# Optimization experiments

Hardware: AMD Instinct MI355X
Metric: run time of the kernel (lower is better)

Reference implementation:

```python
import jax, jax.numpy as jnp
import numpy as np


def _gaussian_kernel(k=3, mu=0.0, sigma=1.0):
    g1 = np.linspace(-1, 1, k)
    x, y = np.meshgrid(g1, g1)
    d = np.sqrt(x ** 2 + y ** 2)
    g = np.exp(-(d - mu) ** 2 / (2 * sigma ** 2)) / (2 * np.pi * sigma ** 2)
    return (g / g.sum()).astype(np.float32)


def _sobel_kernel(k=3):
    r = np.linspace(-(k // 2), k // 2, k)
    x, y = np.meshgrid(r, r)
    den = x ** 2 + y ** 2
    den[:, k // 2] = 1
    return (x / den).astype(np.float32)


def _thin_kernels():
    # 8 directional NMS kernels: +1 at center, -1 at the neighbor rotated by 45*i deg
    # (matches cv2.getRotationMatrix2D + warpAffine(NEAREST) + crop + diag mask).
    ks = []
    for i in range(8):
        th = np.deg2rad(45.0 * i)
        dx = int(np.round(np.cos(th)))
        dy = int(np.round(-np.sin(th)))  # image coords: y down
        k = np.zeros((3, 3), np.float32)
        k[1, 1] = 1.0
        k[1 + dy, 1 + dx] = -1.0
        ks.append(k)
    return np.stack(ks)  # [8,3,3]


def _conv(x, w, pad, groups=1):
    return jax.lax.conv_general_dilated(
        x, w, window_strides=(1, 1), padding=[(pad, pad), (pad, pad)],
        dimension_numbers=('NCHW', 'OIHW', 'NCHW'), feature_group_count=groups)


def setup_inputs() -> dict:
    key = jax.random.key(0)
    B, C, H, W = 16, 3, 512, 512
    img = jax.random.normal(key, (B, C, H, W), dtype=jnp.float32)
    w_gauss = jnp.asarray(_gaussian_kernel(3, 0.0, 1.0))[None, None]          # [1,1,3,3]
    sob = _sobel_kernel(3)
    w_sobel_x = jnp.asarray(sob)[None, None]                                  # [1,1,3,3]
    w_sobel_y = jnp.asarray(sob.T)[None, None]                                # [1,1,3,3]
    w_dir = jnp.asarray(_thin_kernels())[:, None]                             # [8,1,3,3]
    return {"img": img, "w_gauss": w_gauss, "w_sobel_x": w_sobel_x,
            "w_sobel_y": w_sobel_y, "w_dir": w_dir}


def reference(img, w_gauss, w_sobel_x, w_sobel_y, w_dir):
    alpha = 0.0
    B, C, H, W = img.shape
    # per-channel gaussian blur (replication pad) == depthwise conv
    img_pad = jnp.pad(img, ((0, 0), (0, 0), (1, 1), (1, 1)), mode='edge')
    blurred = _conv(img_pad, jnp.tile(w_gauss, (C, 1, 1, 1)), 0, groups=C)    # [B,C,H,W]
    # sobel gradients: weight repeated over C -> sums channels, then / C
    pb = jnp.pad(blurred, ((0, 0), (0, 0), (1, 1), (1, 1)), mode='edge')
    gx = _conv(pb, jnp.tile(w_sobel_x, (1, C, 1, 1)), 0) / C                  # [B,1,H,W]
    gy = _conv(pb, jnp.tile(w_sobel_y, (1, C, 1, 1)), 0) / C
    mag = jnp.sqrt(gx ** 2 + gy ** 2)
    orient = jnp.arctan(gy / gx) * (360.0 / np.pi) + 180.0
    orient = jnp.round(orient / 45.0) * 45.0
    mag = jnp.where(mag < alpha, 0.0, mag)
    directional = _conv(mag, w_dir, 1)                                        # [B,8,H,W]
    pos_idx = (orient / 45.0) % 8                                             # [B,1,H,W]
    remove = jnp.zeros(mag.shape, dtype=bool)
    for i in range(4):
        oriented = (pos_idx == i) | (pos_idx == i + 4)
        is_max = jnp.minimum(directional[:, i:i + 1], directional[:, i + 4:i + 5]) > 0.0
        remove = remove | (oriented & ~is_max)
    thin_edges = jnp.where(remove, 0.0, mag)
    return thin_edges
```

## Files before the change

kernel.cpp:

```cpp
#include <hip/hip_runtime.h>
#include <math.h>

#define BB 16
#define CC 3
#define HH 512
#define WW 512
#define CH (HH * WW)

#define SEG 32
#define ROWS (SEG + 6)
#define RING 8
#define NSEG (HH / SEG)
#define OUTW 58
#define NSTRIP 9
#define NT 64
#define NBLOCKS (NSTRIP * NSEG * BB)

#define P1 0.19891237f
#define P2 0.66817864f
#define P3 1.4966058f
#define P4 5.0273395f

__global__ __launch_bounds__(NT) void canny_wave_kernel(
    const float* __restrict__ img,
    const float* __restrict__ wg,
    const float* __restrict__ wsx,
    const float* __restrict__ wsy,
    float* __restrict__ out)
{
    const int lane = threadIdx.x;
    const int wid  = blockIdx.x;

    const int batch = wid / (NSTRIP * NSEG);
    const int rrem  = wid - batch * (NSTRIP * NSEG);
    const int strip = rrem / NSEG;
    const int seg   = rrem - strip * NSEG;
    const int t0    = seg * SEG;
    const int a     = strip * OUTW;
    const int c     = a - 3 + lane;
    const int ccl   = min(max(c, 0), WW - 1);

    const float* imgb = img + (size_t)batch * (CC * CH);
    float* outb = out + (size_t)batch * CH;

    float q0[RING], q1[RING], q2[RING];
#pragma unroll
    for (int k = 0; k < RING; ++k) {
        const float* p = imgb + min(max(t0 - 3 + k, 0), HH - 1) * WW;
        q0[k] = p[ccl];
        q1[k] = (p + CH)[ccl];
        q2[k] = (p + 2 * CH)[ccl];
    }

    const float hb0 = wg[3], hb1 = wg[4], hb2 = wg[5];
    const float hv0 = wg[1] / wg[4], hv2 = wg[7] / wg[4];
    const float sx3 = wsx[3], sx5 = wsx[5];
    const float sx2 = wsx[2], sxc = wsx[5], sx8 = wsx[8];
    const float sy6 = wsy[6], sy7 = wsy[7], sy8 = wsy[8];
    const float sy1 = wsy[1], sy7v = wsy[7];

    const bool isc0   = (c == 0);
    const bool isc511 = (c == WW - 1);
    const bool storem = (lane >= 3) && (lane <= 60) && (c < WW);

    float H0 = 0.f, H1 = 0.f, H2 = 0.f;
    float rxA = 0.f, rxB = 0.f, rxC = 0.f;
    float ryA = 0.f, ryB = 0.f, ryC = 0.f;
    float mUL = 0.f, mUC = 0.f, mUR = 0.f;
    float mCL = 0.f, mCC = 0.f, mCR = 0.f;
    float mDL = 0.f, mDC = 0.f, mDR = 0.f;
    int dC = 0, dD = 0;

#pragma unroll
    for (int k = 0; k < ROWS; ++k) {
        const int s = k & (RING - 1);
        float v = (q0[s] + q1[s]) + q2[s];

        if (k + RING < ROWS) {
            const float* p = imgb + min(max(t0 - 3 + k + RING, 0), HH - 1) * WW;
            q0[s] = p[ccl];
            q1[s] = (p + CH)[ccl];
            q2[s] = (p + 2 * CH)[ccl];
        }

        float vL = __shfl_up(v, 1, 64);
        float vR = __shfl_down(v, 1, 64);
        H0 = H1; H1 = H2;
        H2 = fmaf(hb0, vL, fmaf(hb2, vR, hb1 * v));

        if (k >= 2) {
            float B = fmaf(hv0, H0, fmaf(hv2, H2, H1));
            float BL = __shfl_up(B, 1, 64);   if (isc0)   BL = B;
            float BR = __shfl_down(B, 1, 64); if (isc511) BR = B;
            rxA = rxB; rxB = rxC;
            rxC = fmaf(sx3, BL, sx5 * BR);
            ryA = ryB; ryB = ryC;
            ryC = fmaf(sy6, BL, fmaf(sy8, BR, sy7 * B));
        }

        if (k >= 4) {
            int m = t0 - 5 + k;
            float xa = rxA, xc = rxC, ya = ryA, yc = ryC;
            if (m == 0)      { xa = rxB; ya = ryB; }
            if (m == HH - 1) { xc = rxB; yc = ryB; }
            float gx = fmaf(sx2, xa, fmaf(sx8, xc, sxc * rxB));
            float gy = fmaf(sy1, ya, sy7v * yc);
            float mag = sqrtf(fmaf(gx, gx, gy * gy)) * (1.0f / 3.0f);
            float t = gy * __builtin_amdgcn_rcpf(gx);
            float u = fabsf(t);
            int s4 = (u > P1) + (u > P2) + (u > P3) + (u > P4);
            int dir = ((t < 0.0f) ? (4 - s4) : s4) & 3;
            if (m < 0 || m >= HH) { mag = 0.0f; dir = 0; }
            float nL = __shfl_up(mag, 1, 64);   if (isc0)   nL = 0.0f;
            float nR = __shfl_down(mag, 1, 64); if (isc511) nR = 0.0f;
            mUL = mCL; mUC = mCC; mUR = mCR;
            mCL = mDL; mCC = mDC; mCR = mDR;
            mDL = nL;  mDC = mag; mDR = nR;
            dC = dD; dD = dir;
        }

        if (k >= 6) {
            int o = t0 - 6 + k;
            float n1 = (dC == 0) ? mCR : (dC == 1) ? mUR : (dC == 2) ? mUC : mUL;
            float n2 = (dC == 0) ? mCL : (dC == 1) ? mDL : (dC == 2) ? mDC : mDR;
            float res = (mCC > n1 && mCC > n2) ? mCC : 0.0f;
            if (storem) outb[(size_t)o * WW + c] = res;
        }
    }
}

extern "C" void kernel_launch(void* const* d_in, const int* in_sizes, int n_in,
                              void* d_out, int out_size, void* d_ws, size_t ws_size,
                              hipStream_t stream) {
    const float* img = (const float*)d_in[0];
    const float* wg  = (const float*)d_in[1];
    const float* wsx = (const float*)d_in[2];
    const float* wsy = (const float*)d_in[3];
    float* out = (float*)d_out;

    canny_wave_kernel<<<NBLOCKS, NT, 0, stream>>>(img, wg, wsx, wsy, out);
}
```

Baseline: 101.1 us.

## Process two columns per lane with float2 loads and halve row segments

Each lane now handles two adjacent columns using float2 loads and stores, so a 64-lane wave covers 120 output columns instead of 58. Segment height drops from 32 to 16 rows and the ring buffer from 8 to 6. The wider strips cut halo overhead in the column direction and the count of shuffles per output, but shorter segments raise the 6-row vertical halo overhead. The direction classification now runs on the stored ratio at the NMS stage, which raises register pressure.

```diff
diff --git a/kernel.cpp b/kernel.cpp
--- a/kernel.cpp
+++ b/kernel.cpp
@@ -7,12 +7,12 @@
 #define WW 512
 #define CH (HH * WW)
 
-#define SEG 32
+#define SEG 16
 #define ROWS (SEG + 6)
-#define RING 8
+#define RING 6
 #define NSEG (HH / SEG)
-#define OUTW 58
-#define NSTRIP 9
+#define OUTW 120
+#define NSTRIP 5
 #define NT 64
 #define NBLOCKS (NSTRIP * NSEG * BB)
 
@@ -21,7 +21,7 @@
 #define P3 1.4966058f
 #define P4 5.0273395f
 
-__global__ __launch_bounds__(NT) void canny_wave_kernel(
+__global__ __launch_bounds__(NT) void canny_wave2_kernel(
     const float* __restrict__ img,
     const float* __restrict__ wg,
     const float* __restrict__ wsx,
@@ -33,23 +33,30 @@
 
     const int batch = wid / (NSTRIP * NSEG);
     const int rrem  = wid - batch * (NSTRIP * NSEG);
-    const int strip = rrem / NSEG;
-    const int seg   = rrem - strip * NSEG;
+    const int strip = rrem >> 5;
+    const int seg   = rrem & (NSEG - 1);
     const int t0    = seg * SEG;
     const int a     = strip * OUTW;
-    const int c     = a - 3 + lane;
-    const int ccl   = min(max(c, 0), WW - 1);
+    const int c0    = a - 4 + 2 * lane;
+    const int scl   = min(max(c0, 0), WW - 2);
+
+    const bool eS   = (strip == 0) || (strip == NSTRIP - 1);
+    const bool fixL = (strip == 0) && (c0 < 0);
+    const bool fixR = (strip == NSTRIP - 1) && (c0 >= WW);
+    const bool padL = (strip == 0) && (lane == 2);
+    const bool padR = (strip == NSTRIP - 1) && (lane == 17);
+    const bool storem = (lane >= 2) && (lane <= 61) && (c0 < WW);
 
     const float* imgb = img + (size_t)batch * (CC * CH);
     float* outb = out + (size_t)batch * CH;
 
-    float q0[RING], q1[RING], q2[RING];
+    float2 q0[RING], q1[RING], q2[RING];
 #pragma unroll
     for (int k = 0; k < RING; ++k) {
-        const float* p = imgb + min(max(t0 - 3 + k, 0), HH - 1) * WW;
-        q0[k] = p[ccl];
-        q1[k] = (p + CH)[ccl];
-        q2[k] = (p + 2 * CH)[ccl];
+        const int ro = min(max(t0 - 3 + k, 0), HH - 1) * WW;
+        q0[k] = *(const float2*)(imgb + ro + scl);
+        q1[k] = *(const float2*)(imgb + CH + ro + scl);
+        q2[k] = *(const float2*)(imgb + 2 * CH + ro + scl);
     }
 
     const float hb0 = wg[3], hb1 = wg[4], hb2 = wg[5];
@@ -59,72 +66,109 @@
     const float sy6 = wsy[6], sy7 = wsy[7], sy8 = wsy[8];
     const float sy1 = wsy[1], sy7v = wsy[7];
 
-    const bool isc0   = (c == 0);
-    const bool isc511 = (c == WW - 1);
-    const bool storem = (lane >= 3) && (lane <= 60) && (c < WW);
-
-    float H0 = 0.f, H1 = 0.f, H2 = 0.f;
-    float rxA = 0.f, rxB = 0.f, rxC = 0.f;
-    float ryA = 0.f, ryB = 0.f, ryC = 0.f;
-    float mUL = 0.f, mUC = 0.f, mUR = 0.f;
-    float mCL = 0.f, mCC = 0.f, mCR = 0.f;
-    float mDL = 0.f, mDC = 0.f, mDR = 0.f;
-    int dC = 0, dD = 0;
+    float2 H0 = {0,0}, H1 = {0,0}, H2 = {0,0};
+    float2 rxA = {0,0}, rxB = {0,0}, rxC = {0,0};
+    float2 ryA = {0,0}, ryB = {0,0}, ryC = {0,0};
+    float2 mU = {0,0}, mC = {0,0}, mD = {0,0};
+    float  lU = 0, lC = 0, lD = 0;
+    float  rU = 0, rC = 0, rD = 0;
+    float2 tC = {0,0}, tD = {0,0};
 
 #pragma unroll
     for (int k = 0; k < ROWS; ++k) {
-        const int s = k & (RING - 1);
-        float v = (q0[s] + q1[s]) + q2[s];
+        const int s = k % RING;
+        float2 v;
+        v.x = (q0[s].x + q1[s].x) + q2[s].x;
+        v.y = (q0[s].y + q1[s].y) + q2[s].y;
+        if (eS) {
+            if (fixL) v.y = v.x;
+            if (fixR) v.x = v.y;
+        }
 
         if (k + RING < ROWS) {
-            const float* p = imgb + min(max(t0 - 3 + k + RING, 0), HH - 1) * WW;
-            q0[s] = p[ccl];
-            q1[s] = (p + CH)[ccl];
-            q2[s] = (p + 2 * CH)[ccl];
+            const int ro = min(max(t0 - 3 + k + RING, 0), HH - 1) * WW;
+            q0[s] = *(const float2*)(imgb + ro + scl);
+            q1[s] = *(const float2*)(imgb + CH + ro + scl);
+            q2[s] = *(const float2*)(imgb + 2 * CH + ro + scl);
         }
 
-        float vL = __shfl_up(v, 1, 64);
-        float vR = __shfl_down(v, 1, 64);
+        float vLx = __shfl_up(v.y, 1, 64);
+        float vRx = __shfl_down(v.x, 1, 64);
         H0 = H1; H1 = H2;
-        H2 = fmaf(hb0, vL, fmaf(hb2, vR, hb1 * v));
+        H2.x = fmaf(hb0, vLx, fmaf(hb2, v.y, hb1 * v.x));
+        H2.y = fmaf(hb0, v.x, fmaf(hb2, vRx, hb1 * v.y));
 
         if (k >= 2) {
-            float B = fmaf(hv0, H0, fmaf(hv2, H2, H1));
-            float BL = __shfl_up(B, 1, 64);   if (isc0)   BL = B;
-            float BR = __shfl_down(B, 1, 64); if (isc511) BR = B;
+            float2 B;
+            B.x = fmaf(hv0, H0.x, fmaf(hv2, H2.x, H1.x));
+            B.y = fmaf(hv0, H0.y, fmaf(hv2, H2.y, H1.y));
+            float BLx = __shfl_up(B.y, 1, 64);
+            float BRx = __shfl_down(B.x, 1, 64);
+            if (eS) {
+                if (padL) BLx = B.x;
+                if (padR) BRx = B.y;
+            }
             rxA = rxB; rxB = rxC;
-            rxC = fmaf(sx3, BL, sx5 * BR);
+            rxC.x = fmaf(sx3, BLx, sx5 * B.y);
+            rxC.y = fmaf(sx3, B.x, sx5 * BRx);
             ryA = ryB; ryB = ryC;
-            ryC = fmaf(sy6, BL, fmaf(sy8, BR, sy7 * B));
+            ryC.x = fmaf(sy6, BLx, fmaf(sy8, B.y, sy7 * B.x));
+            ryC.y = fmaf(sy6, B.x, fmaf(sy8, BRx, sy7 * B.y));
         }
 
         if (k >= 4) {
             int m = t0 - 5 + k;
-            float xa = rxA, xc = rxC, ya = ryA, yc = ryC;
+            float2 xa = rxA, xc = rxC, ya = ryA, yc = ryC;
             if (m == 0)      { xa = rxB; ya = ryB; }
             if (m == HH - 1) { xc = rxB; yc = ryB; }
-            float gx = fmaf(sx2, xa, fmaf(sx8, xc, sxc * rxB));
-            float gy = fmaf(sy1, ya, sy7v * yc);
-            float mag = sqrtf(fmaf(gx, gx, gy * gy)) * (1.0f / 3.0f);
-            float t = gy * __builtin_amdgcn_rcpf(gx);
-            float u = fabsf(t);
-            int s4 = (u > P1) + (u > P2) + (u > P3) + (u > P4);
-            int dir = ((t < 0.0f) ? (4 - s4) : s4) & 3;
-            if (m < 0 || m >= HH) { mag = 0.0f; dir = 0; }
-            float nL = __shfl_up(mag, 1, 64);   if (isc0)   nL = 0.0f;
-            float nR = __shfl_down(mag, 1, 64); if (isc511) nR = 0.0f;
-            mUL = mCL; mUC = mCC; mUR = mCR;
-            mCL = mDL; mCC = mDC; mCR = mDR;
-            mDL = nL;  mDC = mag; mDR = nR;
-            dC = dD; dD = dir;
+            float2 gx, gy, M, T;
+            gx.x = fmaf(sx2, xa.x, fmaf(sx8, xc.x, sxc * rxB.x));
+            gx.y = fmaf(sx2, xa.y, fmaf(sx8, xc.y, sxc * rxB.y));
+            gy.x = fmaf(sy1, ya.x, sy7v * yc.x);
+            gy.y = fmaf(sy1, ya.y, sy7v * yc.y);
+            M.x = sqrtf(fmaf(gx.x, gx.x, gy.x * gy.x)) * (1.0f / 3.0f);
+            M.y = sqrtf(fmaf(gx.y, gx.y, gy.y * gy.y)) * (1.0f / 3.0f);
+            T.x = gy.x * __builtin_amdgcn_rcpf(gx.x);
+            T.y = gy.y * __builtin_amdgcn_rcpf(gx.y);
+            if (m < 0 || m >= HH) { M.x = 0.0f; M.y = 0.0f; }
+            float nLx = __shfl_up(M.y, 1, 64);
+            float nRx = __shfl_down(M.x, 1, 64);
+            if (eS) {
+                if (padL) nLx = 0.0f;
+                if (padR) nRx = 0.0f;
+            }
+            mU = mC; lU = lC; rU = rC;
+            mC = mD; lC = lD; rC = rD;
+            mD = M;  lD = nLx; rD = nRx;
+            tC = tD; tD = T;
         }
 
         if (k >= 6) {
-            int o = t0 - 6 + k;
-            float n1 = (dC == 0) ? mCR : (dC == 1) ? mUR : (dC == 2) ? mUC : mUL;
-            float n2 = (dC == 0) ? mCL : (dC == 1) ? mDL : (dC == 2) ? mDC : mDR;
-            float res = (mCC > n1 && mCC > n2) ? mCC : 0.0f;
-            if (storem) outb[(size_t)o * WW + c] = res;
+            float2 res;
+            {
+                float u = fabsf(tC.x);
+                bool c1 = u > P1, c2 = u > P2, c3 = u > P3, c4 = u > P4;
+                bool neg = tC.x < 0.0f;
+                bool horiz = (!c1) || c4;
+                bool vert  = c2 && (!c3);
+                bool diagA = (c1 && (!c2) && (!neg)) || (c3 && (!c4) && neg);
+                float n1 = horiz ? mC.y : (vert ? mU.x : (diagA ? mU.y : lU));
+                float n2 = horiz ? lC   : (vert ? mD.x : (diagA ? lD   : mD.y));
+                res.x = (mC.x > n1 && mC.x > n2) ? mC.x : 0.0f;
+            }
+            {
+                float u = fabsf(tC.y);
+                bool c1 = u > P1, c2 = u > P2, c3 = u > P3, c4 = u > P4;
+                bool neg = tC.y < 0.0f;
+                bool horiz = (!c1) || c4;
+                bool vert  = c2 && (!c3);
+                bool diagA = (c1 && (!c2) && (!neg)) || (c3 && (!c4) && neg);
+                float n1 = horiz ? rC   : (vert ? mU.y : (diagA ? rU   : mU.x));
+                float n2 = horiz ? mC.x : (vert ? mD.y : (diagA ? mD.x : rD));
+                res.y = (mC.y > n1 && mC.y > n2) ? mC.y : 0.0f;
+            }
+            if (storem)
+                *(float2*)(outb + (size_t)(t0 - 6 + k) * WW + c0) = res;
         }
     }
 }
@@ -138,5 +182,5 @@
     const float* wsy = (const float*)d_in[3];
     float* out = (float*)d_out;
 
-    canny_wave_kernel<<<NBLOCKS, NT, 0, stream>>>(img, wg, wsx, wsy, out);
+    canny_wave2_kernel<<<NBLOCKS, NT, 0, stream>>>(img, wg, wsx, wsy, out);
 }
```

Measured after the change: 100.6 us. About the same (-0.5%).
